# Kernel tuning notes

Hardware: AMD Instinct MI355X
Metric: run time of the kernel (lower is better)

## Reference

```python
import jax, jax.numpy as jnp
import numpy as np

B, S, FEAT = 4, 512, 16
D, H, L, DFF, NC, RPH = 512, 8, 6, 2048, 12, 64
DH = D // H
CLAMP = 5.0
LN_EPS = 1e-5
STD_EPS = 1e-6


def setup_inputs() -> dict:
    key = jax.random.key(0)
    ks = iter(jax.random.split(key, 32))
    sc = lambda *shape: 0.02 * jax.random.normal(next(ks), shape, dtype=jnp.float32)
    inp = {
        "x": jax.random.normal(next(ks), (B, S, FEAT), dtype=jnp.float32),
        # RelPosBias2D MLP: Linear(2,RPH) -> ReLU -> Linear(RPH,H)
        "relpos_w1": sc(RPH, 2), "relpos_b1": jnp.zeros((RPH,), jnp.float32),
        "relpos_w2": sc(H, RPH), "relpos_b2": jnp.zeros((H,), jnp.float32),
        "embed_w": sc(D, FEAT), "embed_b": jnp.zeros((D,), jnp.float32),
        # per-layer params stacked on leading L axis
        "attn_in_w": sc(L, 3 * D, D), "attn_in_b": jnp.zeros((L, 3 * D), jnp.float32),
        "attn_out_w": sc(L, D, D), "attn_out_b": jnp.zeros((L, D), jnp.float32),
        "ff_w1": sc(L, DFF, D), "ff_b1": jnp.zeros((L, DFF), jnp.float32),
        "ff_w2": sc(L, D, DFF), "ff_b2": jnp.zeros((L, D), jnp.float32),
        "ln1_s": jnp.ones((L, D), jnp.float32), "ln1_b": jnp.zeros((L, D), jnp.float32),
        "ln2_s": jnp.ones((L, D), jnp.float32), "ln2_b": jnp.zeros((L, D), jnp.float32),
        "fc_w": sc(NC, D), "fc_b": jnp.zeros((NC,), jnp.float32),
    }
    return inp


def _standardize(v):  # (B,S), unmasked path of _masked_standardize
    mean = v.mean(axis=1, keepdims=True)
    var = ((v - mean) ** 2).mean(axis=1, keepdims=True)
    return (v - mean) / jnp.sqrt(var + STD_EPS)


def _layernorm(v, s, b):
    mean = v.mean(axis=-1, keepdims=True)
    var = ((v - mean) ** 2).mean(axis=-1, keepdims=True)
    return (v - mean) * jax.lax.rsqrt(var + LN_EPS) * s + b


def reference(x, relpos_w1, relpos_b1, relpos_w2, relpos_b2, embed_w, embed_b,
              attn_in_w, attn_in_b, attn_out_w, attn_out_b,
              ff_w1, ff_b1, ff_w2, ff_b2, ln1_s, ln1_b, ln2_s, ln2_b, fc_w, fc_b):
    # --- 2D relative position bias ---
    t = _standardize(x[..., 0])
    f = _standardize(x[..., 1])
    dt = t[:, :, None] - t[:, None, :]          # (B,S,S)
    df = f[:, :, None] - f[:, None, :]
    rel = jnp.stack([dt, df], axis=-1)           # (B,S,S,2)
    hid = jax.nn.relu(rel @ relpos_w1.T + relpos_b1)
    bias = hid @ relpos_w2.T + relpos_b2         # (B,S,S,H)
    bias = jnp.clip(bias, -CLAMP, CLAMP)
    bias = jnp.transpose(bias, (0, 3, 1, 2))     # (B,H,S,S)

    h = x @ embed_w.T + embed_b                  # (B,S,D)
    scale = 1.0 / jnp.sqrt(jnp.float32(DH))
    for l in range(L):
        qkv = h @ attn_in_w[l].T + attn_in_b[l]  # (B,S,3D)
        q, k, v = jnp.split(qkv, 3, axis=-1)
        q = q.reshape(B, S, H, DH)
        k = k.reshape(B, S, H, DH)
        v = v.reshape(B, S, H, DH)
        scores = jnp.einsum('bihd,bjhd->bhij', q, k) * scale + bias
        attn = jax.nn.softmax(scores, axis=-1)
        o = jnp.einsum('bhij,bjhd->bihd', attn, v).reshape(B, S, D)
        o = o @ attn_out_w[l].T + attn_out_b[l]
        h = _layernorm(h + o, ln1_s[l], ln1_b[l])
        ff = jax.nn.relu(h @ ff_w1[l].T + ff_b1[l]) @ ff_w2[l].T + ff_b2[l]
        h = _layernorm(h + ff, ln2_s[l], ln2_b[l])

    rep = h.mean(axis=1)                         # mean pooling, no mask
    return rep @ fc_w.T + fc_b                   # (B,NC)
```

## Files before the change

### kernel.cpp

```cpp
#include <hip/hip_runtime.h>
#include <hip/hip_bf16.h>
#include <stdint.h>

using short8 = __attribute__((ext_vector_type(8))) short;
using us4    = __attribute__((ext_vector_type(4))) unsigned short;
using f32x4  = __attribute__((ext_vector_type(4))) float;
using bf16   = __hip_bfloat16;

constexpr int CB=4, CS=512, CF=16, CD=512, CH=8, CL=6, CDFF=2048, CNC=12, CRPH=64, CDH=64;

__device__ inline void gload_lds16(const void* g, void* l) {
    __builtin_amdgcn_global_load_lds((const __attribute__((address_space(1))) void*)g,
                                     (__attribute__((address_space(3))) void*)l, 16, 0, 0);
}
__device__ inline float bfbits2f(unsigned short u) {
    return __uint_as_float(((uint32_t)u) << 16);
}
__device__ inline unsigned short f2bfbits(float f) {
    return __builtin_bit_cast(unsigned short, __float2bfloat16(f));
}

template<int BM, int BN>
__device__ inline void stage_tile(const bf16* A, int lda, const bf16* W, int ldw, int k0,
                                  char* As, char* Bs) {
    constexpr int AC = BM/32, BC = BN/32;
    const int tid = threadIdx.x;
#pragma unroll
    for (int i = 0; i < AC; i++) {
        int s = i*256 + tid;
        int r = s >> 3, u = s & 7;
        const char* gp = (const char*)(A + (size_t)r*lda + k0) + ((u ^ (r&7))*16);
        gload_lds16(gp, As + (size_t)(s & ~63)*16);
    }
#pragma unroll
    for (int i = 0; i < BC; i++) {
        int s = i*256 + tid;
        int r = s >> 3, u = s & 7;
        const char* gp = (const char*)(W + (size_t)r*ldw + k0) + ((u ^ (r&7))*16);
        gload_lds16(gp, Bs + (size_t)(s & ~63)*16);
    }
}

template<int BM, int BN>
__device__ inline void compute_tile64(const char* As, const char* Bs,
                                      int wr, int wc, int c, int g,
                                      f32x4 (&acc)[BM/32][BN/32]) {
    constexpr int MR = BM/32, NR = BN/32;
#pragma unroll
    for (int kk = 0; kk < 2; kk++) {
        short8 af[MR], bfv[NR];
#pragma unroll
        for (int m = 0; m < MR; m++) {
            int row = wr*(BM/2) + m*16 + c;
            af[m] = *(const short8*)(As + row*128 + (((kk*4+g) ^ (row&7))*16));
        }
#pragma unroll
        for (int n = 0; n < NR; n++) {
            int row = wc*(BN/2) + n*16 + c;
            bfv[n] = *(const short8*)(Bs + row*128 + (((kk*4+g) ^ (row&7))*16));
        }
#pragma unroll
        for (int m = 0; m < MR; m++)
#pragma unroll
            for (int n = 0; n < NR; n++)
                acc[m][n] = __builtin_amdgcn_mfma_f32_16x16x32_bf16(af[m], bfv[n], acc[m][n], 0, 0, 0);
    }
}

template<int BM, int BN>
__device__ inline void mm_core_pipe(const bf16* A, int lda, const bf16* W, int ldw, int K,
                                    char* smem, f32x4 (&acc)[BM/32][BN/32]) {
    constexpr int NLD = (BM+BN)/32;
    const int tid = threadIdx.x;
    const int lane = tid & 63, wv = tid >> 6;
    const int wr = wv >> 1, wc = wv & 1;
    const int g = lane >> 4, c = lane & 15;
    char* Ac = smem;                 char* Bc = smem + BM*128;
    char* An = smem + (BM+BN)*128;   char* Bn = An + BM*128;

    stage_tile<BM,BN>(A, lda, W, ldw, 0, Ac, Bc);
    const int nk = K >> 6;
    for (int t = 0; t < nk; t++) {
        if (t + 1 < nk) {
            stage_tile<BM,BN>(A, lda, W, ldw, (t+1)*64, An, Bn);
            asm volatile("s_waitcnt vmcnt(%0)" :: "n"(NLD) : "memory");
        } else {
            asm volatile("s_waitcnt vmcnt(0)" ::: "memory");
        }
        __builtin_amdgcn_s_barrier();
        compute_tile64<BM,BN>(Ac, Bc, wr, wc, c, g, acc);
        __builtin_amdgcn_s_barrier();
        char* tp;
        tp = Ac; Ac = An; An = tp;
        tp = Bc; Bc = Bn; Bn = tp;
    }
}

template<int BM, int BN, int EPI, int KSPLIT>
__global__ __launch_bounds__(256) void k_mm(const bf16* __restrict__ A, int lda,
                                            const bf16* __restrict__ W, int ldw,
                                            const float* __restrict__ bias,
                                            bf16* __restrict__ Cb, float* __restrict__ Cf,
                                            int ldc, int K) {
    __shared__ char smem[2*(BM+BN)*128];
    const int bm = blockIdx.y * BM, bn = blockIdx.x * BN;
    const int kz = (KSPLIT > 1) ? blockIdx.z : 0;
    const int Kper = K / KSPLIT;
    f32x4 acc[BM/32][BN/32] = {};
    mm_core_pipe<BM,BN>(A + (size_t)bm*lda + kz*Kper, lda,
                        W + (size_t)bn*ldw + kz*Kper, ldw, Kper, smem, acc);
    const int lane = threadIdx.x & 63;
    const int wv = threadIdx.x >> 6, wr = wv>>1, wc = wv&1;
    float* Cfz = Cf + (size_t)kz * 2048 * ldc;
#pragma unroll
    for (int m = 0; m < BM/32; m++)
#pragma unroll
        for (int n = 0; n < BN/32; n++)
#pragma unroll
            for (int j = 0; j < 4; j++) {
                int row = bm + wr*(BM/2) + m*16 + (lane>>4)*4 + j;
                int col = bn + wc*(BN/2) + n*16 + (lane&15);
                float v = acc[m][n][j] + ((kz == 0) ? bias[col] : 0.0f);
                if (EPI == 1) v = fmaxf(v, 0.0f);
                if (EPI == 2) Cfz[(size_t)row*ldc + col] = v;
                else          Cb[(size_t)row*ldc + col] = __float2bfloat16(v);
            }
}

__global__ __launch_bounds__(256) void k_mm_qkv(const bf16* __restrict__ A,
                                                const bf16* __restrict__ W,
                                                const float* __restrict__ bias,
                                                bf16* __restrict__ qkvb,
                                                bf16* __restrict__ vtb) {
    constexpr int BM = 128, BN = 128;
    __shared__ char smem[2*(BM+BN)*128];
    const int bm = blockIdx.y * BM, bn = blockIdx.x * BN;
    f32x4 acc[4][4] = {};
    mm_core_pipe<BM,BN>(A + (size_t)bm*CD, CD, W + (size_t)bn*CD, CD, CD, smem, acc);
    const int lane = threadIdx.x & 63;
    const int wv = threadIdx.x >> 6, wr = wv>>1, wc = wv&1;
    const int g = lane >> 4, c = lane & 15;
    if (bn < 2*CD) {
#pragma unroll
        for (int m = 0; m < 4; m++)
#pragma unroll
            for (int n = 0; n < 4; n++)
#pragma unroll
                for (int j = 0; j < 4; j++) {
                    int row = bm + wr*64 + m*16 + g*4 + j;
                    int col = bn + wc*64 + n*16 + c;
                    qkvb[(size_t)row*(3*CD) + col] = __float2bfloat16(acc[m][n][j] + bias[col]);
                }
    } else {
#pragma unroll
        for (int m = 0; m < 4; m++)
#pragma unroll
            for (int n = 0; n < 4; n++) {
                int row0 = bm + wr*64 + m*16 + g*4;
                int col  = bn + wc*64 + n*16 + c;
                int z = (row0 >> 9)*8 + ((col - 2*CD) >> 6);
                int d = (col - 2*CD) & 63;
                int s0 = row0 & 511;
                float bcol = bias[col];
                us4 o;
#pragma unroll
                for (int j = 0; j < 4; j++) o[j] = f2bfbits(acc[m][n][j] + bcol);
                *(us4*)(vtb + ((size_t)z*CDH + d)*CS + s0) = o;
            }
    }
}

__global__ __launch_bounds__(256) void k_attn_fused(const bf16* __restrict__ qkv,
                                                    const bf16* __restrict__ vt,
                                                    const bf16* __restrict__ bias,
                                                    bf16* __restrict__ att) {
    __shared__ char Kbuf[2][16384];
    __shared__ char Vbuf[2][16384];
    __shared__ char Ps[16384];

    const int z = blockIdx.y, b = z >> 3, h = z & 7;
    const int qbase = blockIdx.x * 64;
    const int tid = threadIdx.x, l = tid & 63, w = tid >> 6;
    const int g = l >> 4, c = l & 15, swz = l & 7;
    const int q_global = qbase + w*16 + c;

    const bf16* qrow = qkv + ((size_t)(b*CS + q_global))*(3*CD) + h*CDH;
    short8 bq0 = *(const short8*)(qrow + g*8);
    short8 bq1 = *(const short8*)(qrow + 32 + g*8);
    const bf16* brow = bias + ((size_t)z*CS + q_global)*CS;

    float mrun = -1e30f, lsum = 0.0f;
    f32x4 accO[4] = {};
    char* Pb = Ps + w*4096;

    auto stageKV = [&](int kv0, char* Ks, char* Vs) {
#pragma unroll
        for (int i = 0; i < 4; i++) {
            int s = i*256 + tid;
            int r = s >> 3, u = s & 7;
            const bf16* gk = qkv + ((size_t)(b*CS + kv0 + r))*(3*CD) + CD + h*CDH + ((u ^ (r&7)) * 8);
            gload_lds16(gk, Ks + (size_t)(s & ~63)*16);
        }
#pragma unroll
        for (int i = 0; i < 4; i++) {
            int s = i*256 + tid;
            int d = s >> 4, u = s & 15;
            const bf16* gv = vt + ((size_t)(z*CDH + d))*CS + kv0 + ((u ^ (d&7)) * 8);
            gload_lds16(gv, Vs + (size_t)(s & ~63)*16);
        }
    };

    char* Kc = Kbuf[0]; char* Vc = Vbuf[0];
    char* Kn = Kbuf[1]; char* Vn = Vbuf[1];
    stageKV(0, Kc, Vc);

    for (int t = 0; t < 4; t++) {
        int kv0 = t * 128;
        if (t < 3) {
            stageKV(kv0 + 128, Kn, Vn);
            asm volatile("s_waitcnt vmcnt(8)" ::: "memory");
        } else {
            asm volatile("s_waitcnt vmcnt(0)" ::: "memory");
        }
        __builtin_amdgcn_s_barrier();

        float sv[8][4];
        float tmax = -1e30f;
#pragma unroll
        for (int n = 0; n < 8; n++) {
            int row = n*16 + c;
            short8 af0 = *(const short8*)(Kc + row*128 + ((g    ^ swz) * 16));
            short8 af1 = *(const short8*)(Kc + row*128 + (((4+g) ^ swz) * 16));
            f32x4 a = {};
            a = __builtin_amdgcn_mfma_f32_16x16x32_bf16(af0, bq0, a, 0, 0, 0);
            a = __builtin_amdgcn_mfma_f32_16x16x32_bf16(af1, bq1, a, 0, 0, 0);
            us4 b4 = *(const us4*)(brow + kv0 + n*16 + g*4);
#pragma unroll
            for (int j = 0; j < 4; j++) {
                sv[n][j] = a[j] * 0.125f + bfbits2f(b4[j]);
                tmax = fmaxf(tmax, sv[n][j]);
            }
        }
        tmax = fmaxf(tmax, __shfl_xor(tmax, 16));
        tmax = fmaxf(tmax, __shfl_xor(tmax, 32));
        float mnew = fmaxf(mrun, tmax);
        float corr = __expf(mrun - mnew);
        float tsum = 0.0f;
#pragma unroll
        for (int n = 0; n < 8; n++)
#pragma unroll
            for (int j = 0; j < 4; j++) {
                float e = __expf(sv[n][j] - mnew);
                sv[n][j] = e;
                tsum += e;
            }
        tsum += __shfl_xor(tsum, 16);
        tsum += __shfl_xor(tsum, 32);
        lsum = lsum * corr + tsum;
        mrun = mnew;
#pragma unroll
        for (int n2 = 0; n2 < 4; n2++)
#pragma unroll
            for (int j = 0; j < 4; j++) accO[n2][j] *= corr;

#pragma unroll
        for (int n = 0; n < 8; n++) {
            us4 pk;
#pragma unroll
            for (int j = 0; j < 4; j++) pk[j] = f2bfbits(sv[n][j]);
            *(us4*)(Pb + c*256 + ((n*32 + g*8) ^ (swz << 4))) = pk;
        }

#pragma unroll
        for (int n2 = 0; n2 < 4; n2++) {
            int d = n2*16 + c;
#pragma unroll
            for (int kk = 0; kk < 4; kk++) {
                short8 av = *(const short8*)(Vc + d*256 + (((kk*4 + g) ^ swz) * 16));
                short8 bp = *(const short8*)(Pb + c*256 + (((kk*64 + g*16) ^ (swz << 4))));
                accO[n2] = __builtin_amdgcn_mfma_f32_16x16x32_bf16(av, bp, accO[n2], 0, 0, 0);
            }
        }
        __builtin_amdgcn_s_barrier();
        char* tp;
        tp = Kc; Kc = Kn; Kn = tp;
        tp = Vc; Vc = Vn; Vn = tp;
    }

    float inv = 1.0f / lsum;
    bf16* orow = att + ((size_t)(b*CS + q_global))*CD + h*CDH;
#pragma unroll
    for (int n2 = 0; n2 < 4; n2++) {
        us4 o;
#pragma unroll
        for (int j = 0; j < 4; j++) o[j] = f2bfbits(accO[n2][j] * inv);
        *(us4*)(orow + n2*16 + g*4) = o;
    }
}

__global__ void k_standardize(const float* __restrict__ x, float* __restrict__ ts,
                              float* __restrict__ fs) {
    int b = blockIdx.x, ch = blockIdx.y, tid = threadIdx.x;
    __shared__ float red[256];
    float v0 = x[(b*CS + tid)*CF + ch];
    float v1 = x[(b*CS + tid + 256)*CF + ch];
    red[tid] = v0 + v1; __syncthreads();
    for (int w = 128; w > 0; w >>= 1) { if (tid < w) red[tid] += red[tid+w]; __syncthreads(); }
    float mean = red[0] * (1.0f/CS); __syncthreads();
    float d0 = v0-mean, d1 = v1-mean;
    red[tid] = d0*d0 + d1*d1; __syncthreads();
    for (int w = 128; w > 0; w >>= 1) { if (tid < w) red[tid] += red[tid+w]; __syncthreads(); }
    float inv = rsqrtf(red[0]*(1.0f/CS) + 1e-6f);
    float* o = ch == 0 ? ts : fs;
    o[b*CS + tid] = d0*inv; o[b*CS + tid + 256] = d1*inv;
}

__global__ __launch_bounds__(256) void k_relpos(const float* __restrict__ ts, const float* __restrict__ fs,
                         const float* __restrict__ w1, const float* __restrict__ b1,
                         const float* __restrict__ w2, const float* __restrict__ b2,
                         bf16* __restrict__ bias) {
    int idx = blockIdx.x * 256 + threadIdx.x;
    int j = idx & (CS-1), i = (idx >> 9) & (CS-1), b = idx >> 18;
    float dt = ts[b*CS + i] - ts[b*CS + j];
    float df = fs[b*CS + i] - fs[b*CS + j];
    float acc[CH];
#pragma unroll
    for (int h = 0; h < CH; h++) acc[h] = b2[h];
    for (int r = 0; r < CRPH; r++) {
        float hd = fmaxf(w1[r*2]*dt + w1[r*2+1]*df + b1[r], 0.0f);
#pragma unroll
        for (int h = 0; h < CH; h++) acc[h] += w2[h*CRPH + r] * hd;
    }
#pragma unroll
    for (int h = 0; h < CH; h++) {
        float v = fminf(fmaxf(acc[h], -5.0f), 5.0f);
        bias[((size_t)(b*CH + h)*CS + i)*CS + j] = __float2bfloat16(v);
    }
}

__global__ __launch_bounds__(256) void k_embed(const float* __restrict__ x, const float* __restrict__ w,
                        const float* __restrict__ bv, float* __restrict__ h, bf16* __restrict__ hb) {
    int idx = blockIdx.x * 256 + threadIdx.x;
    int d = idx & (CD-1), m = idx >> 9;
    const float* xr = x + m*CF;
    const float* wr = w + d*CF;
    float acc = bv[d];
#pragma unroll
    for (int f = 0; f < CF; f++) acc += xr[f]*wr[f];
    h[idx] = acc; hb[idx] = __float2bfloat16(acc);
}

template<int NADD>
__global__ __launch_bounds__(256) void k_ln(float* __restrict__ h, const float* __restrict__ a0,
                     const float* __restrict__ a1,
                     const float* __restrict__ s, const float* __restrict__ bv, bf16* __restrict__ hb) {
    int row = blockIdx.x, tid = threadIdx.x;
    __shared__ float red[256];
    size_t i0 = (size_t)row*CD + tid, i1 = i0 + 256;
    float v0 = h[i0] + a0[i0];
    float v1 = h[i1] + a0[i1];
    if (NADD == 2) { v0 += a1[i0]; v1 += a1[i1]; }
    red[tid] = v0 + v1; __syncthreads();
    for (int w = 128; w > 0; w >>= 1) { if (tid < w) red[tid] += red[tid+w]; __syncthreads(); }
    float mean = red[0] * (1.0f/CD); __syncthreads();
    float d0 = v0-mean, d1 = v1-mean;
    red[tid] = d0*d0 + d1*d1; __syncthreads();
    for (int w = 128; w > 0; w >>= 1) { if (tid < w) red[tid] += red[tid+w]; __syncthreads(); }
    float inv = rsqrtf(red[0]*(1.0f/CD) + 1e-5f);
    float o0 = d0*inv*s[tid] + bv[tid];
    float o1 = d1*inv*s[tid+256] + bv[tid+256];
    h[i0] = o0; hb[i0] = __float2bfloat16(o0);
    h[i1] = o1; hb[i1] = __float2bfloat16(o1);
}

__global__ __launch_bounds__(256) void k_wconv(const float* __restrict__ a0, const float* __restrict__ a1,
                        const float* __restrict__ a2, const float* __restrict__ a3,
                        bf16* __restrict__ dst) {
    size_t i = ((size_t)blockIdx.x * 256 + threadIdx.x) * 8;
    const float* src; size_t off;
    if (i < 786432)       { src = a0; off = i; }
    else if (i < 1048576) { src = a1; off = i - 786432; }
    else if (i < 2097152) { src = a2; off = i - 1048576; }
    else                  { src = a3; off = i - 2097152; }
    short8 o;
#pragma unroll
    for (int j = 0; j < 8; j++) o[j] = __builtin_bit_cast(short, __float2bfloat16(src[off + j]));
    *(short8*)(void*)(dst + i) = o;
}

__global__ __launch_bounds__(256) void k_wconv_all(const float* __restrict__ aiw, const float* __restrict__ aow,
                        const float* __restrict__ f1w, const float* __restrict__ f2w,
                        bf16* __restrict__ dst) {
    int lyr = blockIdx.y;
    size_t i = ((size_t)blockIdx.x * 256 + threadIdx.x) * 8;
    const float* src; size_t off;
    if (i < 786432)       { src = aiw + (size_t)lyr* 786432; off = i; }
    else if (i < 1048576) { src = aow + (size_t)lyr* 262144; off = i - 786432; }
    else if (i < 2097152) { src = f1w + (size_t)lyr*1048576; off = i - 1048576; }
    else                  { src = f2w + (size_t)lyr*1048576; off = i - 2097152; }
    short8 o;
#pragma unroll
    for (int j = 0; j < 8; j++) o[j] = __builtin_bit_cast(short, __float2bfloat16(src[off + j]));
    *(short8*)(void*)(dst + (size_t)lyr*3145728 + i) = o;
}

__global__ __launch_bounds__(256) void k_pool(const float* __restrict__ h, float* __restrict__ rep) {
    int b = blockIdx.x, d0 = blockIdx.y * 64;
    int t = threadIdx.x, dl = t & 63, sg = t >> 6;
    float acc = 0.0f;
    for (int s = sg*128; s < sg*128 + 128; s++)
        acc += h[((size_t)(b*CS + s))*CD + d0 + dl];
    __shared__ float red[256];
    red[t] = acc; __syncthreads();
    if (t < 64)
        rep[b*CD + d0 + dl] = (red[t] + red[t+64] + red[t+128] + red[t+192]) * (1.0f/CS);
}

__global__ void k_fc(const float* __restrict__ rep, const float* __restrict__ fcw,
                     const float* __restrict__ fcb, float* __restrict__ out) {
    int b = blockIdx.x, cc = blockIdx.y, l = threadIdx.x;
    float acc = 0.0f;
    for (int d = l; d < CD; d += 64) acc += rep[b*CD + d] * fcw[cc*CD + d];
    for (int o = 32; o > 0; o >>= 1) acc += __shfl_xor(acc, o);
    if (l == 0) out[b*CNC + cc] = acc + fcb[cc];
}

extern "C" void kernel_launch(void* const* d_in, const int* in_sizes, int n_in,
                              void* d_out, int out_size, void* d_ws, size_t ws_size,
                              hipStream_t stream) {
    const float* x   = (const float*)d_in[0];
    const float* rw1 = (const float*)d_in[1];
    const float* rb1 = (const float*)d_in[2];
    const float* rw2 = (const float*)d_in[3];
    const float* rb2 = (const float*)d_in[4];
    const float* emw = (const float*)d_in[5];
    const float* emb = (const float*)d_in[6];
    const float* aiw = (const float*)d_in[7];
    const float* aib = (const float*)d_in[8];
    const float* aow = (const float*)d_in[9];
    const float* aob = (const float*)d_in[10];
    const float* f1w = (const float*)d_in[11];
    const float* f1b = (const float*)d_in[12];
    const float* f2w = (const float*)d_in[13];
    const float* f2b = (const float*)d_in[14];
    const float* l1s = (const float*)d_in[15];
    const float* l1b = (const float*)d_in[16];
    const float* l2s = (const float*)d_in[17];
    const float* l2b = (const float*)d_in[18];
    const float* fcw = (const float*)d_in[19];
    const float* fcb = (const float*)d_in[20];
    float* out = (float*)d_out;

    char* p = (char*)d_ws;
    auto alloc = [&](size_t bytes) { char* r = p; p += (bytes + 255) & ~(size_t)255; return r; };
    bf16*  biasb = (bf16*)alloc((size_t)CB*CH*CS*CS*2);
    float* h     = (float*)alloc((size_t)CB*CS*CD*4);
    bf16*  hb    = (bf16*)alloc((size_t)CB*CS*CD*2);
    bf16*  qkvb  = (bf16*)alloc((size_t)CB*CS*3*CD*2);
    bf16*  vtb   = (bf16*)alloc((size_t)CB*CH*CDH*CS*2);
    bf16*  attb  = (bf16*)alloc((size_t)CB*CS*CD*2);
    float* tmp   = (float*)alloc((size_t)2*CB*CS*CD*4);
    bf16*  ffb   = (bf16*)alloc((size_t)CB*CS*CDFF*2);
    bf16*  wl    = (bf16*)alloc((size_t)3145728*2);
    float* rep   = (float*)alloc((size_t)CB*CD*4);
    float* ts    = (float*)alloc(CB*CS*4);
    float* fs    = (float*)alloc(CB*CS*4);

    size_t used = (size_t)(p - (char*)d_ws);
    const size_t WLE = 3145728;
    bool oneshot = (ws_size > used) && ((ws_size - used) >= (size_t)CL*WLE*2 + 256);
    bf16* wlall = (bf16*)alloc(oneshot ? (size_t)CL*WLE*2 : 0);

    const int M = CB*CS;
    float* tmp2 = tmp + (size_t)M*CD;

    k_standardize<<<dim3(CB,2), 256, 0, stream>>>(x, ts, fs);
    k_relpos<<<(CB*CS*CS)/256, 256, 0, stream>>>(ts, fs, rw1, rb1, rw2, rb2, biasb);
    k_embed<<<(M*CD)/256, 256, 0, stream>>>(x, emw, emb, h, hb);
    if (oneshot)
        k_wconv_all<<<dim3(1536, CL), 256, 0, stream>>>(aiw, aow, f1w, f2w, wlall);

    for (int l = 0; l < CL; l++) {
        const bf16* wbase = oneshot ? (wlall + (size_t)l*WLE) : wl;
        if (!oneshot)
            k_wconv<<<1536, 256, 0, stream>>>(aiw + (size_t)l*786432, aow + (size_t)l*262144,
                                              f1w + (size_t)l*1048576, f2w + (size_t)l*1048576, wl);
        const bf16* wl_aiw = wbase;
        const bf16* wl_aow = wbase + 786432;
        const bf16* wl_f1w = wbase + 1048576;
        const bf16* wl_f2w = wbase + 2097152;
        k_mm_qkv<<<dim3(12,16), 256, 0, stream>>>(hb, wl_aiw, aib + (size_t)l*3*CD, qkvb, vtb);
        k_attn_fused<<<dim3(CS/64, CB*CH), 256, 0, stream>>>(qkvb, vtb, biasb, attb);
        k_mm<64,64,2,1><<<dim3(8,32), 256, 0, stream>>>(attb, CD, wl_aow, CD,
                                                        aob + (size_t)l*CD, nullptr, tmp, CD, CD);
        k_ln<1><<<M, 256, 0, stream>>>(h, tmp, nullptr, l1s + (size_t)l*CD, l1b + (size_t)l*CD, hb);
        k_mm<128,128,1,1><<<dim3(16,16), 256, 0, stream>>>(hb, CD, wl_f1w, CD,
                                                           f1b + (size_t)l*CDFF, ffb, nullptr, CDFF, CD);
        k_mm<64,64,2,2><<<dim3(8,32,2), 256, 0, stream>>>(ffb, CDFF, wl_f2w, CDFF,
                                                          f2b + (size_t)l*CD, nullptr, tmp, CD, CDFF);
        k_ln<2><<<M, 256, 0, stream>>>(h, tmp, tmp2, l2s + (size_t)l*CD, l2b + (size_t)l*CD, hb);
    }

    k_pool<<<dim3(CB, CD/64), 256, 0, stream>>>(h, rep);
    k_fc<<<dim3(CB, CNC), 64, 0, stream>>>(rep, fcw, fcb, out);
}
```

Before: 482.1 us.

## Use 512-thread GEMM blocks, lazy softmax rescale, and warp-per-row LayerNorm

```diff
diff --git a/kernel.cpp b/kernel.cpp
--- a/kernel.cpp
+++ b/kernel.cpp
@@ -20,75 +20,88 @@
     return __builtin_bit_cast(unsigned short, __float2bfloat16(f));
 }
 
-template<int BM, int BN>
+template<int BM, int BN, int TPB>
+struct MMGeom {
+    static constexpr int WC  = (TPB == 512) ? 4 : 2;
+    static constexpr int WR  = (TPB/64)/WC;
+    static constexpr int RS  = BM/WR;
+    static constexpr int CSP = BN/WC;
+    static constexpr int MR  = RS/16;
+    static constexpr int NR  = CSP/16;
+    static constexpr int NLD = (BM+BN)*128/(TPB*16);
+};
+
+template<int BM, int BN, int TPB>
 __device__ inline void stage_tile(const bf16* A, int lda, const bf16* W, int ldw, int k0,
                                   char* As, char* Bs) {
-    constexpr int AC = BM/32, BC = BN/32;
+    constexpr int AC = (BM*128)/(TPB*16);
+    constexpr int BC = (BN*128)/(TPB*16);
     const int tid = threadIdx.x;
 #pragma unroll
     for (int i = 0; i < AC; i++) {
-        int s = i*256 + tid;
+        int s = i*TPB + tid;
         int r = s >> 3, u = s & 7;
         const char* gp = (const char*)(A + (size_t)r*lda + k0) + ((u ^ (r&7))*16);
         gload_lds16(gp, As + (size_t)(s & ~63)*16);
     }
 #pragma unroll
     for (int i = 0; i < BC; i++) {
-        int s = i*256 + tid;
+        int s = i*TPB + tid;
         int r = s >> 3, u = s & 7;
         const char* gp = (const char*)(W + (size_t)r*ldw + k0) + ((u ^ (r&7))*16);
         gload_lds16(gp, Bs + (size_t)(s & ~63)*16);
     }
 }
 
-template<int BM, int BN>
+template<int BM, int BN, int TPB>
 __device__ inline void compute_tile64(const char* As, const char* Bs,
                                       int wr, int wc, int c, int g,
-                                      f32x4 (&acc)[BM/32][BN/32]) {
-    constexpr int MR = BM/32, NR = BN/32;
+                                      f32x4 (&acc)[MMGeom<BM,BN,TPB>::MR][MMGeom<BM,BN,TPB>::NR]) {
+    using G = MMGeom<BM,BN,TPB>;
 #pragma unroll
     for (int kk = 0; kk < 2; kk++) {
-        short8 af[MR], bfv[NR];
-#pragma unroll
-        for (int m = 0; m < MR; m++) {
-            int row = wr*(BM/2) + m*16 + c;
+        short8 af[G::MR], bfv[G::NR];
+#pragma unroll
+        for (int m = 0; m < G::MR; m++) {
+            int row = wr*G::RS + m*16 + c;
             af[m] = *(const short8*)(As + row*128 + (((kk*4+g) ^ (row&7))*16));
         }
 #pragma unroll
-        for (int n = 0; n < NR; n++) {
-            int row = wc*(BN/2) + n*16 + c;
+        for (int n = 0; n < G::NR; n++) {
+            int row = wc*G::CSP + n*16 + c;
             bfv[n] = *(const short8*)(Bs + row*128 + (((kk*4+g) ^ (row&7))*16));
         }
 #pragma unroll
-        for (int m = 0; m < MR; m++)
-#pragma unroll
-            for (int n = 0; n < NR; n++)
+        for (int m = 0; m < G::MR; m++)
+#pragma unroll
+            for (int n = 0; n < G::NR; n++)
                 acc[m][n] = __builtin_amdgcn_mfma_f32_16x16x32_bf16(af[m], bfv[n], acc[m][n], 0, 0, 0);
     }
 }
 
-template<int BM, int BN>
+template<int BM, int BN, int TPB>
 __device__ inline void mm_core_pipe(const bf16* A, int lda, const bf16* W, int ldw, int K,
-                                    char* smem, f32x4 (&acc)[BM/32][BN/32]) {
-    constexpr int NLD = (BM+BN)/32;
+                                    char* smem,
+                                    f32x4 (&acc)[MMGeom<BM,BN,TPB>::MR][MMGeom<BM,BN,TPB>::NR]) {
+    using G = MMGeom<BM,BN,TPB>;
     const int tid = threadIdx.x;
     const int lane = tid & 63, wv = tid >> 6;
-    const int wr = wv >> 1, wc = wv & 1;
+    const int wr = wv / G::WC, wc = wv % G::WC;
     const int g = lane >> 4, c = lane & 15;
     char* Ac = smem;                 char* Bc = smem + BM*128;
     char* An = smem + (BM+BN)*128;   char* Bn = An + BM*128;
 
-    stage_tile<BM,BN>(A, lda, W, ldw, 0, Ac, Bc);
+    stage_tile<BM,BN,TPB>(A, lda, W, ldw, 0, Ac, Bc);
     const int nk = K >> 6;
     for (int t = 0; t < nk; t++) {
         if (t + 1 < nk) {
-            stage_tile<BM,BN>(A, lda, W, ldw, (t+1)*64, An, Bn);
-            asm volatile("s_waitcnt vmcnt(%0)" :: "n"(NLD) : "memory");
+            stage_tile<BM,BN,TPB>(A, lda, W, ldw, (t+1)*64, An, Bn);
+            asm volatile("s_waitcnt vmcnt(%0)" :: "n"(G::NLD) : "memory");
         } else {
             asm volatile("s_waitcnt vmcnt(0)" ::: "memory");
         }
         __builtin_amdgcn_s_barrier();
-        compute_tile64<BM,BN>(Ac, Bc, wr, wc, c, g, acc);
+        compute_tile64<BM,BN,TPB>(Ac, Bc, wr, wc, c, g, acc);
         __builtin_amdgcn_s_barrier();
         char* tp;
         tp = Ac; Ac = An; An = tp;
@@ -96,30 +109,32 @@
     }
 }
 
-template<int BM, int BN, int EPI, int KSPLIT>
-__global__ __launch_bounds__(256) void k_mm(const bf16* __restrict__ A, int lda,
+template<int BM, int BN, int EPI, int KSPLIT, int TPB>
+__global__ __launch_bounds__(TPB) void k_mm(const bf16* __restrict__ A, int lda,
                                             const bf16* __restrict__ W, int ldw,
                                             const float* __restrict__ bias,
                                             bf16* __restrict__ Cb, float* __restrict__ Cf,
                                             int ldc, int K) {
+    using G = MMGeom<BM,BN,TPB>;
     __shared__ char smem[2*(BM+BN)*128];
     const int bm = blockIdx.y * BM, bn = blockIdx.x * BN;
     const int kz = (KSPLIT > 1) ? blockIdx.z : 0;
     const int Kper = K / KSPLIT;
-    f32x4 acc[BM/32][BN/32] = {};
-    mm_core_pipe<BM,BN>(A + (size_t)bm*lda + kz*Kper, lda,
-                        W + (size_t)bn*ldw + kz*Kper, ldw, Kper, smem, acc);
-    const int lane = threadIdx.x & 63;
-    const int wv = threadIdx.x >> 6, wr = wv>>1, wc = wv&1;
+    f32x4 acc[G::MR][G::NR] = {};
+    mm_core_pipe<BM,BN,TPB>(A + (size_t)bm*lda + kz*Kper, lda,
+                            W + (size_t)bn*ldw + kz*Kper, ldw, Kper, smem, acc);
+    const int lane = threadIdx.x & 63, wv = threadIdx.x >> 6;
+    const int wr = wv / G::WC, wc = wv % G::WC;
+    const int g = lane >> 4, c = lane & 15;
     float* Cfz = Cf + (size_t)kz * 2048 * ldc;
 #pragma unroll
-    for (int m = 0; m < BM/32; m++)
-#pragma unroll
-        for (int n = 0; n < BN/32; n++)
+    for (int m = 0; m < G::MR; m++)
+#pragma unroll
+        for (int n = 0; n < G::NR; n++)
 #pragma unroll
             for (int j = 0; j < 4; j++) {
-                int row = bm + wr*(BM/2) + m*16 + (lane>>4)*4 + j;
-                int col = bn + wc*(BN/2) + n*16 + (lane&15);
+                int row = bm + wr*G::RS + m*16 + g*4 + j;
+                int col = bn + wc*G::CSP + n*16 + c;
                 float v = acc[m][n][j] + ((kz == 0) ? bias[col] : 0.0f);
                 if (EPI == 1) v = fmaxf(v, 0.0f);
                 if (EPI == 2) Cfz[(size_t)row*ldc + col] = v;
@@ -127,37 +142,38 @@
             }
 }
 
-__global__ __launch_bounds__(256) void k_mm_qkv(const bf16* __restrict__ A,
+__global__ __launch_bounds__(512) void k_mm_qkv(const bf16* __restrict__ A,
                                                 const bf16* __restrict__ W,
                                                 const float* __restrict__ bias,
                                                 bf16* __restrict__ qkvb,
                                                 bf16* __restrict__ vtb) {
-    constexpr int BM = 128, BN = 128;
+    constexpr int BM = 128, BN = 128, TPB = 512;
+    using G = MMGeom<BM,BN,TPB>;
     __shared__ char smem[2*(BM+BN)*128];
     const int bm = blockIdx.y * BM, bn = blockIdx.x * BN;
-    f32x4 acc[4][4] = {};
-    mm_core_pipe<BM,BN>(A + (size_t)bm*CD, CD, W + (size_t)bn*CD, CD, CD, smem, acc);
-    const int lane = threadIdx.x & 63;
-    const int wv = threadIdx.x >> 6, wr = wv>>1, wc = wv&1;
+    f32x4 acc[G::MR][G::NR] = {};
+    mm_core_pipe<BM,BN,TPB>(A + (size_t)bm*CD, CD, W + (size_t)bn*CD, CD, CD, smem, acc);
+    const int lane = threadIdx.x & 63, wv = threadIdx.x >> 6;
+    const int wr = wv / G::WC, wc = wv % G::WC;
     const int g = lane >> 4, c = lane & 15;
     if (bn < 2*CD) {
 #pragma unroll
-        for (int m = 0; m < 4; m++)
-#pragma unroll
-            for (int n = 0; n < 4; n++)
+        for (int m = 0; m < G::MR; m++)
+#pragma unroll
+            for (int n = 0; n < G::NR; n++)
 #pragma unroll
                 for (int j = 0; j < 4; j++) {
-                    int row = bm + wr*64 + m*16 + g*4 + j;
-                    int col = bn + wc*64 + n*16 + c;
+                    int row = bm + wr*G::RS + m*16 + g*4 + j;
+                    int col = bn + wc*G::CSP + n*16 + c;
                     qkvb[(size_t)row*(3*CD) + col] = __float2bfloat16(acc[m][n][j] + bias[col]);
                 }
     } else {
 #pragma unroll
-        for (int m = 0; m < 4; m++)
-#pragma unroll
-            for (int n = 0; n < 4; n++) {
-                int row0 = bm + wr*64 + m*16 + g*4;
-                int col  = bn + wc*64 + n*16 + c;
+        for (int m = 0; m < G::MR; m++)
+#pragma unroll
+            for (int n = 0; n < G::NR; n++) {
+                int row0 = bm + wr*G::RS + m*16 + g*4;
+                int col  = bn + wc*G::CSP + n*16 + c;
                 int z = (row0 >> 9)*8 + ((col - 2*CD) >> 6);
                 int d = (col - 2*CD) & 63;
                 int s0 = row0 & 511;
@@ -243,25 +259,28 @@
         }
         tmax = fmaxf(tmax, __shfl_xor(tmax, 16));
         tmax = fmaxf(tmax, __shfl_xor(tmax, 32));
-        float mnew = fmaxf(mrun, tmax);
-        float corr = __expf(mrun - mnew);
+        if (!__all(tmax - mrun <= 8.0f)) {
+            float mnew = fmaxf(mrun, tmax);
+            float corr = __expf(mrun - mnew);
+            lsum *= corr;
+#pragma unroll
+            for (int n2 = 0; n2 < 4; n2++)
+#pragma unroll
+                for (int j = 0; j < 4; j++) accO[n2][j] *= corr;
+            mrun = mnew;
+        }
         float tsum = 0.0f;
 #pragma unroll
         for (int n = 0; n < 8; n++)
 #pragma unroll
             for (int j = 0; j < 4; j++) {
-                float e = __expf(sv[n][j] - mnew);
+                float e = __expf(sv[n][j] - mrun);
                 sv[n][j] = e;
                 tsum += e;
             }
         tsum += __shfl_xor(tsum, 16);
         tsum += __shfl_xor(tsum, 32);
-        lsum = lsum * corr + tsum;
-        mrun = mnew;
-#pragma unroll
-        for (int n2 = 0; n2 < 4; n2++)
-#pragma unroll
-            for (int j = 0; j < 4; j++) accO[n2][j] *= corr;
+        lsum += tsum;
 
 #pragma unroll
         for (int n = 0; n < 8; n++) {
@@ -354,23 +373,50 @@
 __global__ __launch_bounds__(256) void k_ln(float* __restrict__ h, const float* __restrict__ a0,
                      const float* __restrict__ a1,
                      const float* __restrict__ s, const float* __restrict__ bv, bf16* __restrict__ hb) {
-    int row = blockIdx.x, tid = threadIdx.x;
-    __shared__ float red[256];
-    size_t i0 = (size_t)row*CD + tid, i1 = i0 + 256;
-    float v0 = h[i0] + a0[i0];
-    float v1 = h[i1] + a0[i1];
-    if (NADD == 2) { v0 += a1[i0]; v1 += a1[i1]; }
-    red[tid] = v0 + v1; __syncthreads();
-    for (int w = 128; w > 0; w >>= 1) { if (tid < w) red[tid] += red[tid+w]; __syncthreads(); }
-    float mean = red[0] * (1.0f/CD); __syncthreads();
-    float d0 = v0-mean, d1 = v1-mean;
-    red[tid] = d0*d0 + d1*d1; __syncthreads();
-    for (int w = 128; w > 0; w >>= 1) { if (tid < w) red[tid] += red[tid+w]; __syncthreads(); }
-    float inv = rsqrtf(red[0]*(1.0f/CD) + 1e-5f);
-    float o0 = d0*inv*s[tid] + bv[tid];
-    float o1 = d1*inv*s[tid+256] + bv[tid+256];
-    h[i0] = o0; hb[i0] = __float2bfloat16(o0);
-    h[i1] = o1; hb[i1] = __float2bfloat16(o1);
+    const int w = threadIdx.x >> 6, l = threadIdx.x & 63;
+    const int row = blockIdx.x*4 + w;
+    float* hr = h + (size_t)row*CD;
+    const float* ar = a0 + (size_t)row*CD;
+    const float* a1r = (NADD == 2) ? (a1 + (size_t)row*CD) : nullptr;
+
+    float v[8];
+    {
+        float4 h0 = ((const float4*)hr)[l*2],  h1 = ((const float4*)hr)[l*2+1];
+        float4 b0 = ((const float4*)ar)[l*2],  b1 = ((const float4*)ar)[l*2+1];
+        v[0]=h0.x+b0.x; v[1]=h0.y+b0.y; v[2]=h0.z+b0.z; v[3]=h0.w+b0.w;
+        v[4]=h1.x+b1.x; v[5]=h1.y+b1.y; v[6]=h1.z+b1.z; v[7]=h1.w+b1.w;
+        if (NADD == 2) {
+            float4 c0 = ((const float4*)a1r)[l*2], c1 = ((const float4*)a1r)[l*2+1];
+            v[0]+=c0.x; v[1]+=c0.y; v[2]+=c0.z; v[3]+=c0.w;
+            v[4]+=c1.x; v[5]+=c1.y; v[6]+=c1.z; v[7]+=c1.w;
+        }
+    }
+    float sum = 0.f, sq = 0.f;
+#pragma unroll
+    for (int i = 0; i < 8; i++) { sum += v[i]; sq += v[i]*v[i]; }
+#pragma unroll
+    for (int off = 1; off < 64; off <<= 1) {
+        sum += __shfl_xor(sum, off);
+        sq  += __shfl_xor(sq, off);
+    }
+    float mean = sum * (1.0f/CD);
+    float var  = sq * (1.0f/CD) - mean*mean;
+    float rstd = rsqrtf(var + 1e-5f);
+
+    float4 s0 = ((const float4*)s)[l*2],  s1 = ((const float4*)s)[l*2+1];
+    float4 g0 = ((const float4*)bv)[l*2], g1 = ((const float4*)bv)[l*2+1];
+    float o[8];
+    o[0]=(v[0]-mean)*rstd*s0.x+g0.x; o[1]=(v[1]-mean)*rstd*s0.y+g0.y;
+    o[2]=(v[2]-mean)*rstd*s0.z+g0.z; o[3]=(v[3]-mean)*rstd*s0.w+g0.w;
+    o[4]=(v[4]-mean)*rstd*s1.x+g1.x; o[5]=(v[5]-mean)*rstd*s1.y+g1.y;
+    o[6]=(v[6]-mean)*rstd*s1.z+g1.z; o[7]=(v[7]-mean)*rstd*s1.w+g1.w;
+
+    ((float4*)hr)[l*2]   = make_float4(o[0],o[1],o[2],o[3]);
+    ((float4*)hr)[l*2+1] = make_float4(o[4],o[5],o[6],o[7]);
+    short8 ob;
+#pragma unroll
+    for (int i = 0; i < 8; i++) ob[i] = (short)f2bfbits(o[i]);
+    *(short8*)(hb + (size_t)row*CD + l*8) = ob;
 }
 
 __global__ __launch_bounds__(256) void k_wconv(const float* __restrict__ a0, const float* __restrict__ a1,
@@ -489,16 +535,16 @@
         const bf16* wl_aow = wbase + 786432;
         const bf16* wl_f1w = wbase + 1048576;
         const bf16* wl_f2w = wbase + 2097152;
-        k_mm_qkv<<<dim3(12,16), 256, 0, stream>>>(hb, wl_aiw, aib + (size_t)l*3*CD, qkvb, vtb);
+        k_mm_qkv<<<dim3(12,16), 512, 0, stream>>>(hb, wl_aiw, aib + (size_t)l*3*CD, qkvb, vtb);
         k_attn_fused<<<dim3(CS/64, CB*CH), 256, 0, stream>>>(qkvb, vtb, biasb, attb);
-        k_mm<64,64,2,1><<<dim3(8,32), 256, 0, stream>>>(attb, CD, wl_aow, CD,
-                                                        aob + (size_t)l*CD, nullptr, tmp, CD, CD);
-        k_ln<1><<<M, 256, 0, stream>>>(h, tmp, nullptr, l1s + (size_t)l*CD, l1b + (size_t)l*CD, hb);
-        k_mm<128,128,1,1><<<dim3(16,16), 256, 0, stream>>>(hb, CD, wl_f1w, CD,
-                                                           f1b + (size_t)l*CDFF, ffb, nullptr, CDFF, CD);
-        k_mm<64,64,2,2><<<dim3(8,32,2), 256, 0, stream>>>(ffb, CDFF, wl_f2w, CDFF,
-                                                          f2b + (size_t)l*CD, nullptr, tmp, CD, CDFF);
-        k_ln<2><<<M, 256, 0, stream>>>(h, tmp, tmp2, l2s + (size_t)l*CD, l2b + (size_t)l*CD, hb);
+        k_mm<64,64,2,1,512><<<dim3(8,32), 512, 0, stream>>>(attb, CD, wl_aow, CD,
+                                                            aob + (size_t)l*CD, nullptr, tmp, CD, CD);
+        k_ln<1><<<M/4, 256, 0, stream>>>(h, tmp, nullptr, l1s + (size_t)l*CD, l1b + (size_t)l*CD, hb);
+        k_mm<128,128,1,1,512><<<dim3(16,16), 512, 0, stream>>>(hb, CD, wl_f1w, CD,
+                                                               f1b + (size_t)l*CDFF, ffb, nullptr, CDFF, CD);
+        k_mm<64,64,2,2,512><<<dim3(8,32,2), 512, 0, stream>>>(ffb, CDFF, wl_f2w, CDFF,
+                                                              f2b + (size_t)l*CD, nullptr, tmp, CD, CDFF);
+        k_ln<2><<<M/4, 256, 0, stream>>>(h, tmp, tmp2, l2s + (size_t)l*CD, l2b + (size_t)l*CD, hb);
     }
 
     k_pool<<<dim3(CB, CD/64), 256, 0, stream>>>(h, rep);
```

New measurement: 456.9 us. 1.06x faster.
